# Kernel optimization log

Hardware: AMD Instinct MI355X
Metric: run time of the kernel (lower is better)

Reference implementation:

```python
import jax, jax.numpy as jnp
import numpy as np


def setup_inputs() -> dict:
    key = jax.random.key(0)
    k1, k2 = jax.random.split(key)
    B, Q, K, H = 8, 2048, 2048, 128
    out_state = jax.random.normal(k1, (B, Q, H), dtype=jnp.float32)
    history = jax.random.normal(k2, (B, K, H), dtype=jnp.float32)
    return {"out_state": out_state, "history": history}


def reference(out_state, history):
    # tanh pre-activation on queries
    q = jnp.tanh(out_state)                              # [B, Q, H]
    # unscaled QK^T scores
    scores = jnp.einsum("bqh,bkh->bqk", q, history)      # [B, Q, K]
    probs = jax.nn.softmax(scores, axis=2)               # softmax over keys
    attn = jnp.einsum("bqk,bkh->bqh", probs, history)    # [B, Q, H]
    return attn
```

## Files before the change

### kernel.cpp

```cpp
#include <hip/hip_runtime.h>
#include <math.h>


typedef _Float16 half8 __attribute__((ext_vector_type(8)));
typedef _Float16 half4 __attribute__((ext_vector_type(4)));
typedef float    f32x4 __attribute__((ext_vector_type(4)));

#define QQ 2048
#define KK 2048
#define HH 128
#define BM 64
#define BN 64
#define NTILES 32
#define KS_STR 136
#define VT_STR 72
#define PS_STR 72
#define L2E 1.44269504f
#define SPLITS_TARGET 3
#define WS_O_FLOATS   ((size_t)256 * BM * HH)
#define WS_ML_FLOATS  ((size_t)256 * BM)

union U32H { unsigned int u; _Float16 h[2]; };

__launch_bounds__(256, 3)
__global__ void attn_main(const float* __restrict__ out_state,
                          const float* __restrict__ history,
                          float* __restrict__ out,
                          float* __restrict__ ws,
                          int splits) {
    __shared__ _Float16 Ks[BN * KS_STR];
    __shared__ _Float16 Vt[HH * VT_STR];
    __shared__ _Float16 Ps[4][16 * PS_STR];

    const int tid  = threadIdx.x;
    const int wave = tid >> 6;
    const int lane = tid & 63;
    const int quad = lane >> 4;
    const int lc   = lane & 15;

    const int bid  = blockIdx.x;
    const int s    = bid >> 8;
    const int r256 = bid & 255;
    const int b    = r256 >> 5;
    const int qb   = r256 & 31;
    const int m0   = qb * BM;

    const int kt0 = (NTILES * s) / splits;
    const int kt1 = (NTILES * (s + 1)) / splits;

    half8 qf[4];
    {
        const int m = m0 + wave * 16 + lc;
        const float* qrow = out_state + ((size_t)b * QQ + m) * HH;
        #pragma unroll
        for (int s4 = 0; s4 < 4; ++s4) {
            const int h0 = 32 * s4 + quad * 8;
            const float4 a = *(const float4*)(qrow + h0);
            const float4 c = *(const float4*)(qrow + h0 + 4);
            qf[s4][0] = (_Float16)tanhf(a.x); qf[s4][1] = (_Float16)tanhf(a.y);
            qf[s4][2] = (_Float16)tanhf(a.z); qf[s4][3] = (_Float16)tanhf(a.w);
            qf[s4][4] = (_Float16)tanhf(c.x); qf[s4][5] = (_Float16)tanhf(c.y);
            qf[s4][6] = (_Float16)tanhf(c.z); qf[s4][7] = (_Float16)tanhf(c.w);
        }
    }

    const f32x4 zero4 = {0.f, 0.f, 0.f, 0.f};
    f32x4 O[8];
    #pragma unroll
    for (int i = 0; i < 8; ++i) O[i] = zero4;
    f32x4 Osum = zero4;
    float rmax = -3.0e38f;

    const int r0  = tid >> 5;
    const int c4  = (tid & 31) * 4;
    const int h0  = 2 * (tid & 63);
    const int n0t = (tid >> 6) * 16;

    const half8 ones = {(_Float16)1.f,(_Float16)1.f,(_Float16)1.f,(_Float16)1.f,
                        (_Float16)1.f,(_Float16)1.f,(_Float16)1.f,(_Float16)1.f};

    for (int kt = kt0; kt < kt1; ++kt) {
        const int n0 = kt * BN;

        float4 g[8];
        const float* hb = history + ((size_t)b * KK + n0) * HH;
        #pragma unroll
        for (int j = 0; j < 8; ++j)
            g[j] = *(const float4*)(hb + (size_t)(r0 + 8 * j) * HH + c4);

        __syncthreads();
        #pragma unroll
        for (int j = 0; j < 8; ++j) {
            half4 hv;
            hv[0] = (_Float16)g[j].x; hv[1] = (_Float16)g[j].y;
            hv[2] = (_Float16)g[j].z; hv[3] = (_Float16)g[j].w;
            *(half4*)&Ks[(r0 + 8 * j) * KS_STR + c4] = hv;
        }
        __syncthreads();
        {
            half8 ra0, ra1, rb0, rb1;
            #pragma unroll
            for (int i = 0; i < 8; ++i) {
                U32H t; t.u = *(const unsigned int*)&Ks[(n0t + i) * KS_STR + h0];
                ra0[i] = t.h[0]; rb0[i] = t.h[1];
            }
            #pragma unroll
            for (int i = 8; i < 16; ++i) {
                U32H t; t.u = *(const unsigned int*)&Ks[(n0t + i) * KS_STR + h0];
                ra1[i - 8] = t.h[0]; rb1[i - 8] = t.h[1];
            }
            *(half8*)&Vt[(h0    ) * VT_STR + n0t    ] = ra0;
            *(half8*)&Vt[(h0    ) * VT_STR + n0t + 8] = ra1;
            *(half8*)&Vt[(h0 + 1) * VT_STR + n0t    ] = rb0;
            *(half8*)&Vt[(h0 + 1) * VT_STR + n0t + 8] = rb1;
        }
        __syncthreads();

        f32x4 S[4];
        #pragma unroll
        for (int nt = 0; nt < 4; ++nt) {
            f32x4 acc = zero4;
            #pragma unroll
            for (int s4 = 0; s4 < 4; ++s4) {
                half8 kf = *(half8*)&Ks[(nt * 16 + lc) * KS_STR + 32 * s4 + quad * 8];
                acc = __builtin_amdgcn_mfma_f32_16x16x32_f16(kf, qf[s4], acc, 0, 0, 0);
            }
            S[nt] = acc;
        }

        float tmax = S[0][0];
        #pragma unroll
        for (int nt = 0; nt < 4; ++nt)
            #pragma unroll
            for (int r = 0; r < 4; ++r)
                tmax = fmaxf(tmax, S[nt][r]);
        tmax = fmaxf(tmax, __shfl_xor(tmax, 16, 64));
        tmax = fmaxf(tmax, __shfl_xor(tmax, 32, 64));

        const float nm = fmaxf(rmax, tmax);
        const float alpha = exp2f((rmax - nm) * L2E);
        rmax = nm;

        #pragma unroll
        for (int nt = 0; nt < 4; ++nt)
            #pragma unroll
            for (int r = 0; r < 4; ++r)
                S[nt][r] = exp2f((S[nt][r] - nm) * L2E);

        #pragma unroll
        for (int ct = 0; ct < 8; ++ct) O[ct] *= alpha;
        Osum *= alpha;

        #pragma unroll
        for (int nt = 0; nt < 4; ++nt) {
            half4 pv;
            pv[0] = (_Float16)S[nt][0]; pv[1] = (_Float16)S[nt][1];
            pv[2] = (_Float16)S[nt][2]; pv[3] = (_Float16)S[nt][3];
            *(half4*)&Ps[wave][lc * PS_STR + nt * 16 + quad * 4] = pv;
        }

        #pragma unroll
        for (int s2 = 0; s2 < 2; ++s2) {
            half8 pb = *(half8*)&Ps[wave][lc * PS_STR + s2 * 32 + quad * 8];
            Osum = __builtin_amdgcn_mfma_f32_16x16x32_f16(ones, pb, Osum, 0, 0, 0);
            #pragma unroll
            for (int ct = 0; ct < 8; ++ct) {
                half8 vf = *(half8*)&Vt[(ct * 16 + lc) * VT_STR + s2 * 32 + quad * 8];
                O[ct] = __builtin_amdgcn_mfma_f32_16x16x32_f16(vf, pb, O[ct], 0, 0, 0);
            }
        }
    }

    if (splits == 1) {
        const float inv = 1.0f / Osum[0];
        float* orow = out + ((size_t)b * QQ + m0 + wave * 16 + lc) * HH;
        #pragma unroll
        for (int ct = 0; ct < 8; ++ct) {
            f32x4 v = O[ct] * inv;
            *(f32x4*)&orow[ct * 16 + quad * 4] = v;
        }
    } else {
        float* po = ws + ((size_t)(s * 256 + r256)) * (BM * HH) + (wave * 16 + lc) * HH;
        #pragma unroll
        for (int ct = 0; ct < 8; ++ct)
            *(f32x4*)&po[ct * 16 + quad * 4] = O[ct];
        if (quad == 0) {
            const size_t mlBase = (size_t)splits * WS_O_FLOATS;
            const size_t idx = (size_t)(s * 256 + r256) * BM + wave * 16 + lc;
            ws[mlBase + idx] = rmax;
            ws[mlBase + (size_t)splits * WS_ML_FLOATS + idx] = Osum[0];
        }
    }
}

__global__ void attn_combine(const float* __restrict__ ws,
                             float* __restrict__ out,
                             int splits) {
    const int idx = blockIdx.x * 256 + threadIdx.x;
    const int h  = idx & 127;
    const int q  = (idx >> 7) & 2047;
    const int b  = idx >> 18;
    const int qb = q >> 6;
    const int qr = q & 63;
    const int blk = b * 32 + qb;

    const size_t mlBase = (size_t)splits * WS_O_FLOATS;
    const size_t lBase  = mlBase + (size_t)splits * WS_ML_FLOATS;

    float ms[4];
    float M = -3.0e38f;
    for (int s = 0; s < splits; ++s) {
        ms[s] = ws[mlBase + (size_t)(s * 256 + blk) * BM + qr];
        M = fmaxf(M, ms[s]);
    }
    float denom = 0.f, val = 0.f;
    for (int s = 0; s < splits; ++s) {
        const float w = exp2f((ms[s] - M) * L2E);
        denom += w * ws[lBase + (size_t)(s * 256 + blk) * BM + qr];
        val   += w * ws[(size_t)(s * 256 + blk) * (BM * HH) + qr * HH + h];
    }
    out[idx] = val / denom;
}

extern "C" void kernel_launch(void* const* d_in, const int* in_sizes, int n_in,
                              void* d_out, int out_size, void* d_ws, size_t ws_size,
                              hipStream_t stream) {
    const float* out_state = (const float*)d_in[0];
    const float* history   = (const float*)d_in[1];
    float* out = (float*)d_out;
    float* ws  = (float*)d_ws;

    const size_t needed = (size_t)SPLITS_TARGET * (WS_O_FLOATS + 2 * WS_ML_FLOATS) * 4;
    const int splits = (ws_size >= needed) ? SPLITS_TARGET : 1;

    attn_main<<<dim3(256 * splits), dim3(256), 0, stream>>>(out_state, history, out, ws, splits);
    if (splits > 1)
        attn_combine<<<dim3((8 * QQ * HH) / 256), dim3(256), 0, stream>>>(ws, out, splits);
}
```

Before: 117.8 us.

## Fuse split-K combine into main kernel via atomic last-block reduction

Drops the separate combine kernel: each split block writes its partials and bumps an atomic counter per query group, and the last block to arrive merges all splits in place. The split count rises to up to 4 and occupancy to 4 blocks per CU. It also removes the per-wave P staging in shared memory by feeding the S accumulator registers directly into 16x16x16 MFMAs. In exchange it adds a memset launch, thread fences, and a serialized tail of combine work in the last-arriving blocks, and the smaller MFMA shape doubles the instruction count for the PV product.

Result: slower. 268.1 us (+127.6%).

```diff
diff --git a/kernel.cpp b/kernel.cpp
--- a/kernel.cpp
+++ b/kernel.cpp
@@ -14,15 +14,14 @@
 #define NTILES 32
 #define KS_STR 136
 #define VT_STR 72
-#define PS_STR 72
 #define L2E 1.44269504f
-#define SPLITS_TARGET 3
-#define WS_O_FLOATS   ((size_t)256 * BM * HH)
-#define WS_ML_FLOATS  ((size_t)256 * BM)
+#define NGROUPS 256
+#define OSPLIT  ((size_t)NGROUPS * BM * HH)
+#define MLSPLIT ((size_t)NGROUPS * BM)
 
 union U32H { unsigned int u; _Float16 h[2]; };
 
-__launch_bounds__(256, 3)
+__launch_bounds__(256, 4)
 __global__ void attn_main(const float* __restrict__ out_state,
                           const float* __restrict__ history,
                           float* __restrict__ out,
@@ -30,7 +29,7 @@
                           int splits) {
     __shared__ _Float16 Ks[BN * KS_STR];
     __shared__ _Float16 Vt[HH * VT_STR];
-    __shared__ _Float16 Ps[4][16 * PS_STR];
+    __shared__ int lastFlag;
 
     const int tid  = threadIdx.x;
     const int wave = tid >> 6;
@@ -38,12 +37,12 @@
     const int quad = lane >> 4;
     const int lc   = lane & 15;
 
-    const int bid  = blockIdx.x;
-    const int s    = bid >> 8;
-    const int r256 = bid & 255;
-    const int b    = r256 >> 5;
-    const int qb   = r256 & 31;
-    const int m0   = qb * BM;
+    const int bid = blockIdx.x;
+    const int s   = bid >> 8;
+    const int g   = bid & 255;
+    const int b   = g >> 5;
+    const int qb  = g & 31;
+    const int m0  = qb * BM;
 
     const int kt0 = (NTILES * s) / splits;
     const int kt1 = (NTILES * (s + 1)) / splits;
@@ -76,24 +75,23 @@
     const int h0  = 2 * (tid & 63);
     const int n0t = (tid >> 6) * 16;
 
-    const half8 ones = {(_Float16)1.f,(_Float16)1.f,(_Float16)1.f,(_Float16)1.f,
-                        (_Float16)1.f,(_Float16)1.f,(_Float16)1.f,(_Float16)1.f};
+    const half4 ones4 = {(_Float16)1.f, (_Float16)1.f, (_Float16)1.f, (_Float16)1.f};
 
     for (int kt = kt0; kt < kt1; ++kt) {
         const int n0 = kt * BN;
 
-        float4 g[8];
+        float4 gbuf[8];
         const float* hb = history + ((size_t)b * KK + n0) * HH;
         #pragma unroll
         for (int j = 0; j < 8; ++j)
-            g[j] = *(const float4*)(hb + (size_t)(r0 + 8 * j) * HH + c4);
+            gbuf[j] = *(const float4*)(hb + (size_t)(r0 + 8 * j) * HH + c4);
 
         __syncthreads();
         #pragma unroll
         for (int j = 0; j < 8; ++j) {
             half4 hv;
-            hv[0] = (_Float16)g[j].x; hv[1] = (_Float16)g[j].y;
-            hv[2] = (_Float16)g[j].z; hv[3] = (_Float16)g[j].w;
+            hv[0] = (_Float16)gbuf[j].x; hv[1] = (_Float16)gbuf[j].y;
+            hv[2] = (_Float16)gbuf[j].z; hv[3] = (_Float16)gbuf[j].w;
             *(half4*)&Ks[(r0 + 8 * j) * KS_STR + c4] = hv;
         }
         __syncthreads();
@@ -153,20 +151,14 @@
 
         #pragma unroll
         for (int nt = 0; nt < 4; ++nt) {
-            half4 pv;
-            pv[0] = (_Float16)S[nt][0]; pv[1] = (_Float16)S[nt][1];
-            pv[2] = (_Float16)S[nt][2]; pv[3] = (_Float16)S[nt][3];
-            *(half4*)&Ps[wave][lc * PS_STR + nt * 16 + quad * 4] = pv;
-        }
-
-        #pragma unroll
-        for (int s2 = 0; s2 < 2; ++s2) {
-            half8 pb = *(half8*)&Ps[wave][lc * PS_STR + s2 * 32 + quad * 8];
-            Osum = __builtin_amdgcn_mfma_f32_16x16x32_f16(ones, pb, Osum, 0, 0, 0);
+            half4 pb;
+            pb[0] = (_Float16)S[nt][0]; pb[1] = (_Float16)S[nt][1];
+            pb[2] = (_Float16)S[nt][2]; pb[3] = (_Float16)S[nt][3];
+            Osum = __builtin_amdgcn_mfma_f32_16x16x16f16(ones4, pb, Osum, 0, 0, 0);
             #pragma unroll
             for (int ct = 0; ct < 8; ++ct) {
-                half8 vf = *(half8*)&Vt[(ct * 16 + lc) * VT_STR + s2 * 32 + quad * 8];
-                O[ct] = __builtin_amdgcn_mfma_f32_16x16x32_f16(vf, pb, O[ct], 0, 0, 0);
+                half4 af = *(half4*)&Vt[(ct * 16 + lc) * VT_STR + nt * 16 + quad * 4];
+                O[ct] = __builtin_amdgcn_mfma_f32_16x16x16f16(af, pb, O[ct], 0, 0, 0);
             }
         }
     }
@@ -179,47 +171,50 @@
             f32x4 v = O[ct] * inv;
             *(f32x4*)&orow[ct * 16 + quad * 4] = v;
         }
-    } else {
-        float* po = ws + ((size_t)(s * 256 + r256)) * (BM * HH) + (wave * 16 + lc) * HH;
-        #pragma unroll
-        for (int ct = 0; ct < 8; ++ct)
-            *(f32x4*)&po[ct * 16 + quad * 4] = O[ct];
-        if (quad == 0) {
-            const size_t mlBase = (size_t)splits * WS_O_FLOATS;
-            const size_t idx = (size_t)(s * 256 + r256) * BM + wave * 16 + lc;
-            ws[mlBase + idx] = rmax;
-            ws[mlBase + (size_t)splits * WS_ML_FLOATS + idx] = Osum[0];
-        }
-    }
-}
-
-__global__ void attn_combine(const float* __restrict__ ws,
-                             float* __restrict__ out,
-                             int splits) {
-    const int idx = blockIdx.x * 256 + threadIdx.x;
-    const int h  = idx & 127;
-    const int q  = (idx >> 7) & 2047;
-    const int b  = idx >> 18;
-    const int qb = q >> 6;
-    const int qr = q & 63;
-    const int blk = b * 32 + qb;
-
-    const size_t mlBase = (size_t)splits * WS_O_FLOATS;
-    const size_t lBase  = mlBase + (size_t)splits * WS_ML_FLOATS;
-
-    float ms[4];
-    float M = -3.0e38f;
-    for (int s = 0; s < splits; ++s) {
-        ms[s] = ws[mlBase + (size_t)(s * 256 + blk) * BM + qr];
-        M = fmaxf(M, ms[s]);
-    }
-    float denom = 0.f, val = 0.f;
-    for (int s = 0; s < splits; ++s) {
-        const float w = exp2f((ms[s] - M) * L2E);
-        denom += w * ws[lBase + (size_t)(s * 256 + blk) * BM + qr];
-        val   += w * ws[(size_t)(s * 256 + blk) * (BM * HH) + qr * HH + h];
-    }
-    out[idx] = val / denom;
+        return;
+    }
+
+    const size_t mBase = (size_t)splits * OSPLIT;
+    const size_t lBase = mBase + (size_t)splits * MLSPLIT;
+    float* po = ws + ((size_t)s * NGROUPS + g) * (BM * HH) + (wave * 16 + lc) * HH;
+    #pragma unroll
+    for (int ct = 0; ct < 8; ++ct)
+        *(f32x4*)&po[ct * 16 + quad * 4] = O[ct];
+    if (quad == 0) {
+        const size_t idx = (size_t)(s * NGROUPS + g) * BM + wave * 16 + lc;
+        ws[mBase + idx] = rmax;
+        ws[lBase + idx] = Osum[0];
+    }
+
+    __threadfence();
+    if (tid == 0) {
+        unsigned int* cnt = (unsigned int*)(ws + lBase + (size_t)splits * MLSPLIT);
+        unsigned int old = atomicAdd(&cnt[g], 1u);
+        lastFlag = (old == (unsigned int)(splits - 1));
+    }
+    __syncthreads();
+    if (!lastFlag) return;
+    __threadfence();
+
+    const int h4 = (tid & 31) * 4;
+    for (int q = tid >> 5; q < BM; q += 8) {
+        float ms[4];
+        float M = -3.0e38f;
+        for (int sp = 0; sp < splits; ++sp) {
+            ms[sp] = ws[mBase + (size_t)(sp * NGROUPS + g) * BM + q];
+            M = fmaxf(M, ms[sp]);
+        }
+        float denom = 0.f;
+        f32x4 val = {0.f, 0.f, 0.f, 0.f};
+        for (int sp = 0; sp < splits; ++sp) {
+            const float w = exp2f((ms[sp] - M) * L2E);
+            denom += w * ws[lBase + (size_t)(sp * NGROUPS + g) * BM + q];
+            const f32x4 ov = *(const f32x4*)&ws[(size_t)(sp * NGROUPS + g) * (BM * HH) + (size_t)q * HH + h4];
+            val += w * ov;
+        }
+        const float inv = 1.0f / denom;
+        *(f32x4*)&out[((size_t)b * QQ + m0 + q) * HH + h4] = val * inv;
+    }
 }
 
 extern "C" void kernel_launch(void* const* d_in, const int* in_sizes, int n_in,
@@ -230,10 +225,15 @@
     float* out = (float*)d_out;
     float* ws  = (float*)d_ws;
 
-    const size_t needed = (size_t)SPLITS_TARGET * (WS_O_FLOATS + 2 * WS_ML_FLOATS) * 4;
-    const int splits = (ws_size >= needed) ? SPLITS_TARGET : 1;
-
-    attn_main<<<dim3(256 * splits), dim3(256), 0, stream>>>(out_state, history, out, ws, splits);
-    if (splits > 1)
-        attn_combine<<<dim3((8 * QQ * HH) / 256), dim3(256), 0, stream>>>(ws, out, splits);
+    int splits = 1;
+    for (int cand = 4; cand >= 2; --cand) {
+        const size_t bytes = (size_t)cand * (OSPLIT + 2 * MLSPLIT) * 4 + NGROUPS * 4;
+        if (ws_size >= bytes) { splits = cand; break; }
+    }
+
+    if (splits > 1) {
+        const size_t cntOff = (size_t)splits * (OSPLIT + 2 * MLSPLIT) * 4;
+        hipMemsetAsync((char*)d_ws + cntOff, 0, NGROUPS * 4, stream);
+    }
+    attn_main<<<dim3(NGROUPS * splits), dim3(256), 0, stream>>>(out_state, history, out, ws, splits);
 }
```
